# Kernel optimization log

Hardware: AMD Instinct MI355X
Metric: run time of the kernel (lower is better)

## Reference

```python
import jax, jax.numpy as jnp
import numpy as np

B, S, HID, H = 4, 2048, 1024, 16
D = HID // H  # dim per head


def setup_inputs() -> dict:
    key = jax.random.key(0)
    ks = jax.random.split(key, 7)
    inp = {
        "q": jax.random.normal(ks[0], (B, S, HID), dtype=jnp.float32),
        "k": jax.random.normal(ks[1], (B, S, HID), dtype=jnp.float32),
        "v": jax.random.normal(ks[2], (B, S, HID), dtype=jnp.float32),
        # Linear weights stored as (in, out); applied as x @ W. use_bias=False.
        "Wq": jax.random.normal(ks[3], (HID, HID), dtype=jnp.float32) * (1.0 / np.sqrt(HID)),
        "Wk": jax.random.normal(ks[4], (HID, HID), dtype=jnp.float32) * (1.0 / np.sqrt(HID)),
        "Wv": jax.random.normal(ks[5], (HID, HID), dtype=jnp.float32) * (1.0 / np.sqrt(HID)),
        "Wo": jax.random.normal(ks[6], (HID, HID), dtype=jnp.float32) * (1.0 / np.sqrt(HID)),
    }
    return inp


def reference(q, k, v, Wq, Wk, Wv, Wo):
    scale = 1.0 / jnp.sqrt(jnp.float32(D))
    # QKV projections, then split hidden into (H, D) heads (same layout as transpose_qkv)
    Q = (q @ Wq).reshape(B, S, H, D)
    K = (k @ Wk).reshape(B, S, H, D)
    V = (v @ Wv).reshape(B, S, H, D)
    # scaled dot-product attention: full [B,H,S,S] score matrix, softmax over keys
    attn_w = jnp.einsum("bqhd,bkhd->bhqk", Q, K) * scale
    attn_w = jax.nn.softmax(attn_w, axis=-1)
    # dropout rate is 0 (eval-mode / deterministic)
    O = jnp.einsum("bhqk,bkhd->bqhd", attn_w, V).reshape(B, S, HID)
    return O @ Wo
```

## Files before the change

### kernel.cpp

```cpp
#include <hip/hip_runtime.h>


typedef __attribute__((ext_vector_type(8))) short short8;
typedef __attribute__((ext_vector_type(4))) float float4v;

#if __has_builtin(__builtin_amdgcn_exp2f)
#define EXP2F(x) __builtin_amdgcn_exp2f(x)
#else
#define EXP2F(x) exp2f(x)
#endif

__device__ __forceinline__ unsigned short f2b(float x) {
  return (unsigned short)((__float_as_uint(x) + 0x8000u) >> 16);
}
__device__ __forceinline__ unsigned pk2f(float a, float b) {
  unsigned ua = __float_as_uint(a) + 0x8000u;
  unsigned ub = __float_as_uint(b) + 0x8000u;
  return __builtin_amdgcn_perm(ub, ua, 0x07060302);
}

typedef __attribute__((address_space(3))) unsigned int lds_uint;
typedef const __attribute__((address_space(1))) unsigned int gbl_uint;
__device__ __forceinline__ void stage16(const unsigned short* g, unsigned short* l) {
#if __has_builtin(__builtin_amdgcn_global_load_lds)
  __builtin_amdgcn_global_load_lds((gbl_uint*)g, (lds_uint*)l, 16, 0, 0);
#else
  *(uint4*)l = *(const uint4*)g;
#endif
}

__global__ __launch_bounds__(256) void conv_qkv(const float* __restrict__ q,
                                                const float* __restrict__ k,
                                                const float* __restrict__ v,
                                                unsigned short* __restrict__ ws,
                                                float qscale) {
  const int z = blockIdx.y;
  const float* src = z == 0 ? q : (z == 1 ? k : v);
  unsigned short* dst = ws + (size_t)z * 8388608;
  const float s = z == 0 ? qscale : 1.0f;
  size_t i = ((size_t)blockIdx.x * 256 + threadIdx.x) * 8;
  float4v a = *(const float4v*)(src + i);
  float4v b = *(const float4v*)(src + i + 4);
  uint4 o;
  o.x = pk2f(a.x * s, a.y * s);
  o.y = pk2f(a.z * s, a.w * s);
  o.z = pk2f(b.x * s, b.y * s);
  o.w = pk2f(b.z * s, b.w * s);
  *(uint4*)(dst + i) = o;
}

__global__ __launch_bounds__(256) void wtrans(const float* __restrict__ Wq,
                                              const float* __restrict__ Wk,
                                              const float* __restrict__ Wv,
                                              const float* __restrict__ Wo,
                                              unsigned short* __restrict__ Wt) {
  __shared__ float tile[32][33];
  const float* W = blockIdx.z == 0 ? Wq : blockIdx.z == 1 ? Wk
                   : blockIdx.z == 2 ? Wv : Wo;
  unsigned short* T = Wt + (size_t)blockIdx.z * 1048576;
  const int tx = threadIdx.x & 31, ty = threadIdx.x >> 5;
  const int k0 = blockIdx.y * 32, n0 = blockIdx.x * 32;
#pragma unroll
  for (int i = 0; i < 4; i++)
    tile[ty + 8 * i][tx] = W[(size_t)(k0 + ty + 8 * i) * 1024 + n0 + tx];
  __syncthreads();
#pragma unroll
  for (int i = 0; i < 4; i++)
    T[(size_t)(n0 + ty + 8 * i) * 1024 + k0 + tx] = f2b(tile[tx][ty + 8 * i]);
}

template <int MODE, bool SWAP>
__global__ __launch_bounds__(256, 2) void gemm_bt(const unsigned short* __restrict__ A,
                                                  const unsigned short* __restrict__ Bt,
                                                  void* __restrict__ Cg) {
  __shared__ __align__(16) unsigned short As[128 * 64];
  __shared__ __align__(16) unsigned short Bs[128 * 64];
  const int tid = threadIdx.x;
  const int lane = tid & 63;
  const int w = tid >> 6;
  const int quad = lane >> 4, col = lane & 15;
  const int wm = w >> 1, wn = w & 1;
  const int lin = blockIdx.x;
  const int xcd = lin & 7, grp = lin >> 3;
  const int m0 = ((grp & 7) * 8 + xcd) * 128;
  const int n0 = (grp >> 3) * 128;
  const int rA = lane >> 3, cA = lane & 7;

  float4v acc[4][4] = {};

  for (int k0 = 0; k0 < 1024; k0 += 64) {
    __syncthreads();
#pragma unroll
    for (int j = 0; j < 4; j++) {
      const int row = w * 32 + j * 8 + rA;
      stage16(A + (unsigned)(m0 + row) * 1024 + k0 + ((cA ^ rA) * 8),
              &As[row * 64 + cA * 8]);
      stage16(Bt + (unsigned)(n0 + row) * 1024 + k0 + ((cA ^ rA) * 8),
              &Bs[row * 64 + cA * 8]);
    }
    __syncthreads();

#pragma unroll
    for (int ks = 0; ks < 2; ks++) {
      short8 af[4], bf[4];
#pragma unroll
      for (int mi = 0; mi < 4; mi++) {
        int row = wm * 64 + mi * 16 + col;
        af[mi] = *(const short8*)&As[row * 64 + (((ks * 4 + quad) ^ (col & 7)) * 8)];
      }
#pragma unroll
      for (int ni = 0; ni < 4; ni++) {
        int row = wn * 64 + ni * 16 + col;
        bf[ni] = *(const short8*)&Bs[row * 64 + (((ks * 4 + quad) ^ (col & 7)) * 8)];
      }
#pragma unroll
      for (int mi = 0; mi < 4; mi++)
#pragma unroll
        for (int ni = 0; ni < 4; ni++) {
          if (SWAP)
            acc[ni][mi] = __builtin_amdgcn_mfma_f32_16x16x32_bf16(
                bf[ni], af[mi], acc[ni][mi], 0, 0, 0);
          else
            acc[mi][ni] = __builtin_amdgcn_mfma_f32_16x16x32_bf16(
                af[mi], bf[ni], acc[mi][ni], 0, 0, 0);
        }
    }
  }

  if (MODE == 0) {
#pragma unroll
    for (int ni = 0; ni < 4; ni++) {
      const int cg = n0 + wn * 64 + ni * 16 + quad * 4;
      const int h = cg >> 6, dlo = cg & 63;
#pragma unroll
      for (int mi = 0; mi < 4; mi++) {
        const int tok = m0 + wm * 64 + mi * 16 + col;
        const int b = tok >> 11, s = tok & 2047;
        uint2 pk;
        pk.x = pk2f(acc[ni][mi][0], acc[ni][mi][1]);
        pk.y = pk2f(acc[ni][mi][2], acc[ni][mi][3]);
        *(uint2*)((unsigned short*)Cg +
                  ((unsigned)((b * 16 + h) * 2048 + s) * 64 + dlo)) = pk;
      }
    }
  } else if (MODE == 1) {
#pragma unroll
    for (int mi = 0; mi < 4; mi++) {
      const int tok = m0 + wm * 64 + mi * 16 + quad * 4;
      const int b = tok >> 11, s = tok & 2047;
#pragma unroll
      for (int ni = 0; ni < 4; ni++) {
        const int cg = n0 + wn * 64 + ni * 16 + col;
        const int h = cg >> 6, d = cg & 63;
        uint2 pk;
        pk.x = pk2f(acc[mi][ni][0], acc[mi][ni][1]);
        pk.y = pk2f(acc[mi][ni][2], acc[mi][ni][3]);
        *(uint2*)((unsigned short*)Cg +
                  ((unsigned)((b * 16 + h) * 64 + d) * 2048 + s)) = pk;
      }
    }
  } else {
#pragma unroll
    for (int mi = 0; mi < 4; mi++) {
      const int row = m0 + wm * 64 + mi * 16 + quad * 4;
#pragma unroll
      for (int ni = 0; ni < 4; ni++) {
        const int cg = n0 + wn * 64 + ni * 16 + col;
#pragma unroll
        for (int r = 0; r < 4; r++)
          ((float*)Cg)[(unsigned)(row + r) * 1024 + cg] = acc[mi][ni][r];
      }
    }
  }
}

#define PSTR 160
__global__ __launch_bounds__(256, 2) void attn_kernel(
    const unsigned short* __restrict__ Qb, const unsigned short* __restrict__ Kb,
    const unsigned short* __restrict__ Vt, unsigned short* __restrict__ Ob) {
  __shared__ __align__(16) unsigned short K_lds[128 * 64];
  __shared__ __align__(16) unsigned short V_lds[64 * 128];
  __shared__ __align__(16) unsigned short P_lds[128 * PSTR];
  __shared__ float den_lds[128];

  const int tid = threadIdx.x;
  const int lane = tid & 63;
  const int w = tid >> 6;
  const int quad = lane >> 4, col = lane & 15;
  const int wq = w >> 1, wk = w & 1;
  const int lin = blockIdx.x;
  const int bh = ((lin >> 3) & 7) * 8 + (lin & 7);
  const int qt = lin >> 6;

  const unsigned short* Kbase = Kb + (size_t)bh * (2048 * 64);
  const unsigned short* Vbase = Vt + (size_t)bh * (64 * 2048);

  short8 qf[4][2];
#pragma unroll
  for (int qi = 0; qi < 4; qi++)
#pragma unroll
    for (int ks = 0; ks < 2; ks++) {
      int s = qt * 128 + wq * 64 + qi * 16 + col;
      qf[qi][ks] = *(const short8*)(Qb + ((size_t)bh * 2048 + s) * 64 + ks * 32 + quad * 8);
    }

  float4v oacc[2][4] = {};
  float dens[4] = {};

  if (tid < 128) den_lds[tid] = 0.f;

  const int rK = lane >> 3, cK = lane & 7;
  const int rV = lane >> 4, cV = lane & 15;

  for (int kt = 0; kt < 16; kt++) {
    const int s0 = kt * 128;
    __syncthreads();
#pragma unroll
    for (int j = 0; j < 4; j++) {
      const int rowK = w * 32 + j * 8 + rK;
      stage16(Kbase + (unsigned)(s0 + rowK) * 64 + ((cK ^ rK) * 8),
              &K_lds[rowK * 64 + cK * 8]);
      const int rowV = w * 16 + j * 4 + rV;
      stage16(Vbase + (unsigned)rowV * 2048 + s0 + (((cV ^ (rowV & 15)) & 15) * 8),
              &V_lds[rowV * 128 + cV * 8]);
    }
    __syncthreads();

    float4v sacc[4][4] = {};
    short8 kf[4][2];
#pragma unroll
    for (int ki = 0; ki < 4; ki++)
#pragma unroll
      for (int ks = 0; ks < 2; ks++) {
        int row = wk * 64 + ki * 16 + col;
        kf[ki][ks] = *(const short8*)&K_lds[row * 64 +
                                            (((ks * 4 + quad) ^ (col & 7)) * 8)];
      }
#pragma unroll
    for (int ki = 0; ki < 4; ki++)
#pragma unroll
      for (int qi = 0; qi < 4; qi++)
#pragma unroll
        for (int ks = 0; ks < 2; ks++)
          sacc[ki][qi] = __builtin_amdgcn_mfma_f32_16x16x32_bf16(
              kf[ki][ks], qf[qi][ks], sacc[ki][qi], 0, 0, 0);

#pragma unroll
    for (int ki = 0; ki < 4; ki++) {
      const int c = wk * 8 + ki * 2 + (quad >> 1);
      const int hh = quad & 1;
#pragma unroll
      for (int qi = 0; qi < 4; qi++) {
        const int q = wq * 64 + qi * 16 + col;
        float p0 = EXP2F(sacc[ki][qi][0]);
        float p1 = EXP2F(sacc[ki][qi][1]);
        float p2 = EXP2F(sacc[ki][qi][2]);
        float p3 = EXP2F(sacc[ki][qi][3]);
        dens[qi] += (p0 + p1) + (p2 + p3);
        uint2 pk;
        pk.x = pk2f(p0, p1);
        pk.y = pk2f(p2, p3);
        *(uint2*)&P_lds[q * PSTR + ((c ^ col) & 15) * 8 + hh * 4] = pk;
      }
    }
    __syncthreads();

#pragma unroll
    for (int ks = 0; ks < 4; ks++) {
      short8 pf[4], vf[2];
#pragma unroll
      for (int mi = 0; mi < 4; mi++) {
        int row = wq * 64 + mi * 16 + col;
        pf[mi] = *(const short8*)&P_lds[row * PSTR + ((((ks * 4 + quad) ^ col) & 15) * 8)];
      }
#pragma unroll
      for (int nv = 0; nv < 2; nv++) {
        int row = wk * 32 + nv * 16 + col;
        vf[nv] = *(const short8*)&V_lds[row * 128 + ((((ks * 4 + quad) ^ col) & 15) * 8)];
      }
#pragma unroll
      for (int nv = 0; nv < 2; nv++)
#pragma unroll
        for (int mi = 0; mi < 4; mi++)
          oacc[nv][mi] = __builtin_amdgcn_mfma_f32_16x16x32_bf16(
              vf[nv], pf[mi], oacc[nv][mi], 0, 0, 0);
    }
  }

#pragma unroll
  for (int qi = 0; qi < 4; qi++) {
    float v = dens[qi];
    v += __shfl_xor(v, 16);
    v += __shfl_xor(v, 32);
    if (lane < 16) atomicAdd(&den_lds[wq * 64 + qi * 16 + col], v);
  }
  __syncthreads();

  const int b = bh >> 4, h = bh & 15;
#pragma unroll
  for (int mi = 0; mi < 4; mi++) {
    const int srow = qt * 128 + wq * 64 + mi * 16 + col;
    const float rd = 1.f / den_lds[wq * 64 + mi * 16 + col];
    unsigned base = (unsigned)(b * 2048 + srow) * 1024 + h * 64;
#pragma unroll
    for (int nv = 0; nv < 2; nv++) {
      const int d0 = wk * 32 + nv * 16 + quad * 4;
      uint2 pk;
      pk.x = pk2f(oacc[nv][mi][0] * rd, oacc[nv][mi][1] * rd);
      pk.y = pk2f(oacc[nv][mi][2] * rd, oacc[nv][mi][3] * rd);
      *(uint2*)(Ob + base + d0) = pk;
    }
  }
}

extern "C" void kernel_launch(void* const* d_in, const int* in_sizes, int n_in,
                              void* d_out, int out_size, void* d_ws, size_t ws_size,
                              hipStream_t stream) {
  const float* q = (const float*)d_in[0];
  const float* k = (const float*)d_in[1];
  const float* v = (const float*)d_in[2];
  const float* Wq = (const float*)d_in[3];
  const float* Wk = (const float*)d_in[4];
  const float* Wv = (const float*)d_in[5];
  const float* Wo = (const float*)d_in[6];

  unsigned short* ws = (unsigned short*)d_ws;
  unsigned short* qb = ws;
  unsigned short* kb = ws + 8388608;
  unsigned short* vb = ws + 16777216;
  unsigned short* Qb = ws + 25165824;
  unsigned short* Kb = ws + 33554432;
  unsigned short* Vt = ws + 41943040;
  unsigned short* Wt = ws + 50331648;

  dim3 blk(256);
  const float qscale = 0.18033688011112042f;

  conv_qkv<<<dim3(4096, 3), blk, 0, stream>>>(q, k, v, ws, qscale);
  wtrans<<<dim3(32, 32, 4), blk, 0, stream>>>(Wq, Wk, Wv, Wo, Wt);

  gemm_bt<0, true><<<dim3(512), blk, 0, stream>>>(qb, Wt + 0 * 1048576, Qb);
  gemm_bt<0, true><<<dim3(512), blk, 0, stream>>>(kb, Wt + 1 * 1048576, Kb);
  gemm_bt<1, false><<<dim3(512), blk, 0, stream>>>(vb, Wt + 2 * 1048576, Vt);

  attn_kernel<<<dim3(1024), blk, 0, stream>>>(Qb, Kb, Vt, qb );

  gemm_bt<2, false><<<dim3(512), blk, 0, stream>>>(qb , Wt + 3 * 1048576,
                                                   (float*)d_out);
}
```

Before: 350.4 us.

## Rework attention to 32x32 MFMA with register-resident P and fuse QKV GEMMs

```diff
diff --git a/kernel.cpp b/kernel.cpp
--- a/kernel.cpp
+++ b/kernel.cpp
@@ -3,6 +3,7 @@
 
 typedef __attribute__((ext_vector_type(8))) short short8;
 typedef __attribute__((ext_vector_type(4))) float float4v;
+typedef __attribute__((ext_vector_type(16))) float float16v;
 
 #if __has_builtin(__builtin_amdgcn_exp2f)
 #define EXP2F(x) __builtin_amdgcn_exp2f(x)
@@ -69,10 +70,111 @@
     T[(size_t)(n0 + ty + 8 * i) * 1024 + k0 + tx] = f2b(tile[tx][ty + 8 * i]);
 }
 
-template <int MODE, bool SWAP>
-__global__ __launch_bounds__(256, 2) void gemm_bt(const unsigned short* __restrict__ A,
-                                                  const unsigned short* __restrict__ Bt,
-                                                  void* __restrict__ Cg) {
+__global__ __launch_bounds__(256, 3) void gemm_qkv(
+    const unsigned short* __restrict__ qb, const unsigned short* __restrict__ kb,
+    const unsigned short* __restrict__ vb, const unsigned short* __restrict__ Wt,
+    unsigned short* __restrict__ Qb, unsigned short* __restrict__ Kb,
+    unsigned short* __restrict__ Vt) {
+  __shared__ __align__(16) unsigned short As[128 * 64];
+  __shared__ __align__(16) unsigned short Bs[128 * 64];
+  const int tid = threadIdx.x;
+  const int lane = tid & 63;
+  const int w = tid >> 6;
+  const int quad = lane >> 4, col = lane & 15;
+  const int wm = w >> 1, wn = w & 1;
+  const int lin = blockIdx.x;
+  const int z = lin >> 9;
+  const int r = lin & 511;
+  const int xcd = r & 7, grp = r >> 3;
+  const int m0 = ((grp & 7) * 8 + xcd) * 128;
+  const int n0 = (grp >> 3) * 128;
+  const int rA = lane >> 3, cA = lane & 7;
+
+  const unsigned short* A = z == 0 ? qb : (z == 1 ? kb : vb);
+  const unsigned short* Bt = Wt + (unsigned)z * 1048576;
+
+  float4v acc[4][4] = {};
+
+  for (int k0 = 0; k0 < 1024; k0 += 64) {
+    __syncthreads();
+#pragma unroll
+    for (int j = 0; j < 4; j++) {
+      const int row = w * 32 + j * 8 + rA;
+      stage16(A + (unsigned)(m0 + row) * 1024 + k0 + ((cA ^ rA) * 8),
+              &As[row * 64 + cA * 8]);
+      stage16(Bt + (unsigned)(n0 + row) * 1024 + k0 + ((cA ^ rA) * 8),
+              &Bs[row * 64 + cA * 8]);
+    }
+    __syncthreads();
+
+#pragma unroll
+    for (int ks = 0; ks < 2; ks++) {
+      short8 af[4], bf[4];
+#pragma unroll
+      for (int mi = 0; mi < 4; mi++) {
+        int row = wm * 64 + mi * 16 + col;
+        af[mi] = *(const short8*)&As[row * 64 + (((ks * 4 + quad) ^ (col & 7)) * 8)];
+      }
+#pragma unroll
+      for (int ni = 0; ni < 4; ni++) {
+        int row = wn * 64 + ni * 16 + col;
+        bf[ni] = *(const short8*)&Bs[row * 64 + (((ks * 4 + quad) ^ (col & 7)) * 8)];
+      }
+      if (z < 2) {
+#pragma unroll
+        for (int mi = 0; mi < 4; mi++)
+#pragma unroll
+          for (int ni = 0; ni < 4; ni++)
+            acc[ni][mi] = __builtin_amdgcn_mfma_f32_16x16x32_bf16(
+                bf[ni], af[mi], acc[ni][mi], 0, 0, 0);
+      } else {
+#pragma unroll
+        for (int mi = 0; mi < 4; mi++)
+#pragma unroll
+          for (int ni = 0; ni < 4; ni++)
+            acc[mi][ni] = __builtin_amdgcn_mfma_f32_16x16x32_bf16(
+                af[mi], bf[ni], acc[mi][ni], 0, 0, 0);
+      }
+    }
+  }
+
+  if (z < 2) {
+    unsigned short* Cg = z == 0 ? Qb : Kb;
+#pragma unroll
+    for (int ni = 0; ni < 4; ni++) {
+      const int cg = n0 + wn * 64 + ni * 16 + quad * 4;
+      const int h = cg >> 6, dlo = cg & 63;
+#pragma unroll
+      for (int mi = 0; mi < 4; mi++) {
+        const int tok = m0 + wm * 64 + mi * 16 + col;
+        const int b = tok >> 11, s = tok & 2047;
+        uint2 pk;
+        pk.x = pk2f(acc[ni][mi][0], acc[ni][mi][1]);
+        pk.y = pk2f(acc[ni][mi][2], acc[ni][mi][3]);
+        *(uint2*)(Cg + ((unsigned)((b * 16 + h) * 2048 + s) * 64 + dlo)) = pk;
+      }
+    }
+  } else {
+#pragma unroll
+    for (int mi = 0; mi < 4; mi++) {
+      const int tok = m0 + wm * 64 + mi * 16 + quad * 4;
+      const int b = tok >> 11, s = tok & 2047;
+#pragma unroll
+      for (int ni = 0; ni < 4; ni++) {
+        const int cg = n0 + wn * 64 + ni * 16 + col;
+        const int h = cg >> 6, d = cg & 63;
+        uint2 pk;
+        pk.x = pk2f(acc[mi][ni][0], acc[mi][ni][1]);
+        pk.y = pk2f(acc[mi][ni][2], acc[mi][ni][3]);
+        *(uint2*)(Vt + ((unsigned)((b * 16 + h) * 64 + d) * 2048 + s)) = pk;
+      }
+    }
+  }
+}
+
+__global__ __launch_bounds__(256, 2) void gemm_out(const unsigned short* __restrict__ A,
+                                                   const unsigned short* __restrict__ Bt,
+                                                   float* __restrict__ Cg) {
   __shared__ __align__(16) unsigned short As[128 * 64];
   __shared__ __align__(16) unsigned short Bs[128 * 64];
   const int tid = threadIdx.x;
@@ -116,78 +218,37 @@
 #pragma unroll
       for (int mi = 0; mi < 4; mi++)
 #pragma unroll
-        for (int ni = 0; ni < 4; ni++) {
-          if (SWAP)
-            acc[ni][mi] = __builtin_amdgcn_mfma_f32_16x16x32_bf16(
-                bf[ni], af[mi], acc[ni][mi], 0, 0, 0);
-          else
-            acc[mi][ni] = __builtin_amdgcn_mfma_f32_16x16x32_bf16(
-                af[mi], bf[ni], acc[mi][ni], 0, 0, 0);
-        }
-    }
-  }
-
-  if (MODE == 0) {
+        for (int ni = 0; ni < 4; ni++)
+          acc[mi][ni] = __builtin_amdgcn_mfma_f32_16x16x32_bf16(af[mi], bf[ni],
+                                                               acc[mi][ni], 0, 0, 0);
+    }
+  }
+
+#pragma unroll
+  for (int mi = 0; mi < 4; mi++) {
+    const int row = m0 + wm * 64 + mi * 16 + quad * 4;
 #pragma unroll
     for (int ni = 0; ni < 4; ni++) {
-      const int cg = n0 + wn * 64 + ni * 16 + quad * 4;
-      const int h = cg >> 6, dlo = cg & 63;
-#pragma unroll
-      for (int mi = 0; mi < 4; mi++) {
-        const int tok = m0 + wm * 64 + mi * 16 + col;
-        const int b = tok >> 11, s = tok & 2047;
-        uint2 pk;
-        pk.x = pk2f(acc[ni][mi][0], acc[ni][mi][1]);
-        pk.y = pk2f(acc[ni][mi][2], acc[ni][mi][3]);
-        *(uint2*)((unsigned short*)Cg +
-                  ((unsigned)((b * 16 + h) * 2048 + s) * 64 + dlo)) = pk;
-      }
-    }
-  } else if (MODE == 1) {
-#pragma unroll
-    for (int mi = 0; mi < 4; mi++) {
-      const int tok = m0 + wm * 64 + mi * 16 + quad * 4;
-      const int b = tok >> 11, s = tok & 2047;
-#pragma unroll
-      for (int ni = 0; ni < 4; ni++) {
-        const int cg = n0 + wn * 64 + ni * 16 + col;
-        const int h = cg >> 6, d = cg & 63;
-        uint2 pk;
-        pk.x = pk2f(acc[mi][ni][0], acc[mi][ni][1]);
-        pk.y = pk2f(acc[mi][ni][2], acc[mi][ni][3]);
-        *(uint2*)((unsigned short*)Cg +
-                  ((unsigned)((b * 16 + h) * 64 + d) * 2048 + s)) = pk;
-      }
-    }
-  } else {
-#pragma unroll
-    for (int mi = 0; mi < 4; mi++) {
-      const int row = m0 + wm * 64 + mi * 16 + quad * 4;
-#pragma unroll
-      for (int ni = 0; ni < 4; ni++) {
-        const int cg = n0 + wn * 64 + ni * 16 + col;
-#pragma unroll
-        for (int r = 0; r < 4; r++)
-          ((float*)Cg)[(unsigned)(row + r) * 1024 + cg] = acc[mi][ni][r];
-      }
-    }
-  }
-}
-
-#define PSTR 160
-__global__ __launch_bounds__(256, 2) void attn_kernel(
+      const int cg = n0 + wn * 64 + ni * 16 + col;
+#pragma unroll
+      for (int r = 0; r < 4; r++)
+        Cg[(unsigned)(row + r) * 1024 + cg] = acc[mi][ni][r];
+    }
+  }
+}
+
+__global__ __launch_bounds__(256, 3) void attn_kernel(
     const unsigned short* __restrict__ Qb, const unsigned short* __restrict__ Kb,
     const unsigned short* __restrict__ Vt, unsigned short* __restrict__ Ob) {
   __shared__ __align__(16) unsigned short K_lds[128 * 64];
   __shared__ __align__(16) unsigned short V_lds[64 * 128];
-  __shared__ __align__(16) unsigned short P_lds[128 * PSTR];
-  __shared__ float den_lds[128];
 
   const int tid = threadIdx.x;
   const int lane = tid & 63;
   const int w = tid >> 6;
-  const int quad = lane >> 4, col = lane & 15;
-  const int wq = w >> 1, wk = w & 1;
+  const int l31 = lane & 31;
+  const int hl = lane >> 5;
+
   const int lin = blockIdx.x;
   const int bh = ((lin >> 3) & 7) * 8 + (lin & 7);
   const int qt = lin >> 6;
@@ -195,122 +256,108 @@
   const unsigned short* Kbase = Kb + (size_t)bh * (2048 * 64);
   const unsigned short* Vbase = Vt + (size_t)bh * (64 * 2048);
 
-  short8 qf[4][2];
-#pragma unroll
-  for (int qi = 0; qi < 4; qi++)
-#pragma unroll
-    for (int ks = 0; ks < 2; ks++) {
-      int s = qt * 128 + wq * 64 + qi * 16 + col;
-      qf[qi][ks] = *(const short8*)(Qb + ((size_t)bh * 2048 + s) * 64 + ks * 32 + quad * 8);
-    }
-
-  float4v oacc[2][4] = {};
-  float dens[4] = {};
-
-  if (tid < 128) den_lds[tid] = 0.f;
-
-  const int rK = lane >> 3, cK = lane & 7;
-  const int rV = lane >> 4, cV = lane & 15;
+  short8 qf[4];
+  {
+    const int s = qt * 128 + w * 32 + l31;
+    const unsigned short* qrow = Qb + ((size_t)bh * 2048 + s) * 64 + 8 * hl;
+#pragma unroll
+    for (int ks = 0; ks < 4; ks++) qf[ks] = *(const short8*)(qrow + 16 * ks);
+  }
+
+  float16v oacc[2];
+#pragma unroll
+  for (int di = 0; di < 2; di++)
+#pragma unroll
+    for (int e = 0; e < 16; e++) oacc[di][e] = 0.f;
+  float den = 0.f;
+
+  union PF { uint2 u[2]; short8 s8; };
 
   for (int kt = 0; kt < 16; kt++) {
     const int s0 = kt * 128;
     __syncthreads();
 #pragma unroll
-    for (int j = 0; j < 4; j++) {
-      const int rowK = w * 32 + j * 8 + rK;
-      stage16(Kbase + (unsigned)(s0 + rowK) * 64 + ((cK ^ rK) * 8),
-              &K_lds[rowK * 64 + cK * 8]);
-      const int rowV = w * 16 + j * 4 + rV;
-      stage16(Vbase + (unsigned)rowV * 2048 + s0 + (((cV ^ (rowV & 15)) & 15) * 8),
-              &V_lds[rowV * 128 + cV * 8]);
-    }
-    __syncthreads();
-
-    float4v sacc[4][4] = {};
-    short8 kf[4][2];
-#pragma unroll
-    for (int ki = 0; ki < 4; ki++)
-#pragma unroll
-      for (int ks = 0; ks < 2; ks++) {
-        int row = wk * 64 + ki * 16 + col;
-        kf[ki][ks] = *(const short8*)&K_lds[row * 64 +
-                                            (((ks * 4 + quad) ^ (col & 7)) * 8)];
-      }
-#pragma unroll
-    for (int ki = 0; ki < 4; ki++)
-#pragma unroll
-      for (int qi = 0; qi < 4; qi++)
-#pragma unroll
-        for (int ks = 0; ks < 2; ks++)
-          sacc[ki][qi] = __builtin_amdgcn_mfma_f32_16x16x32_bf16(
-              kf[ki][ks], qf[qi][ks], sacc[ki][qi], 0, 0, 0);
-
+    for (int jj = 0; jj < 4; jj++) {
+      {
+        const int row = (w * 4 + jj) * 8 + (lane >> 3);
+        const int cl = (lane & 7) ^ (row & 7);
+        stage16(Kbase + (unsigned)(s0 + row) * 64 + cl * 8,
+                &K_lds[row * 64 + (lane & 7) * 8]);
+      }
+      {
+        const int row = (w * 4 + jj) * 4 + (lane >> 4);
+        const int cl = (lane & 15) ^ (row & 15);
+        stage16(Vbase + (unsigned)row * 2048 + s0 + cl * 8,
+                &V_lds[row * 128 + (lane & 15) * 8]);
+      }
+    }
+    __syncthreads();
+
+    PF pfrag[8];
 #pragma unroll
     for (int ki = 0; ki < 4; ki++) {
-      const int c = wk * 8 + ki * 2 + (quad >> 1);
-      const int hh = quad & 1;
-#pragma unroll
-      for (int qi = 0; qi < 4; qi++) {
-        const int q = wq * 64 + qi * 16 + col;
-        float p0 = EXP2F(sacc[ki][qi][0]);
-        float p1 = EXP2F(sacc[ki][qi][1]);
-        float p2 = EXP2F(sacc[ki][qi][2]);
-        float p3 = EXP2F(sacc[ki][qi][3]);
-        dens[qi] += (p0 + p1) + (p2 + p3);
-        uint2 pk;
-        pk.x = pk2f(p0, p1);
-        pk.y = pk2f(p2, p3);
-        *(uint2*)&P_lds[q * PSTR + ((c ^ col) & 15) * 8 + hh * 4] = pk;
-      }
-    }
-    __syncthreads();
-
-#pragma unroll
-    for (int ks = 0; ks < 4; ks++) {
-      short8 pf[4], vf[2];
-#pragma unroll
-      for (int mi = 0; mi < 4; mi++) {
-        int row = wq * 64 + mi * 16 + col;
-        pf[mi] = *(const short8*)&P_lds[row * PSTR + ((((ks * 4 + quad) ^ col) & 15) * 8)];
-      }
-#pragma unroll
-      for (int nv = 0; nv < 2; nv++) {
-        int row = wk * 32 + nv * 16 + col;
-        vf[nv] = *(const short8*)&V_lds[row * 128 + ((((ks * 4 + quad) ^ col) & 15) * 8)];
-      }
-#pragma unroll
-      for (int nv = 0; nv < 2; nv++)
-#pragma unroll
-        for (int mi = 0; mi < 4; mi++)
-          oacc[nv][mi] = __builtin_amdgcn_mfma_f32_16x16x32_bf16(
-              vf[nv], pf[mi], oacc[nv][mi], 0, 0, 0);
-    }
-  }
-
-#pragma unroll
-  for (int qi = 0; qi < 4; qi++) {
-    float v = dens[qi];
-    v += __shfl_xor(v, 16);
-    v += __shfl_xor(v, 32);
-    if (lane < 16) atomicAdd(&den_lds[wq * 64 + qi * 16 + col], v);
-  }
-  __syncthreads();
+      float16v sacc;
+#pragma unroll
+      for (int e = 0; e < 16; e++) sacc[e] = 0.f;
+#pragma unroll
+      for (int ks = 0; ks < 4; ks++) {
+        const int row = ki * 32 + l31;
+        short8 kfr = *(const short8*)&K_lds[row * 64 +
+                                            (((2 * ks + hl) ^ (row & 7)) * 8)];
+        sacc = __builtin_amdgcn_mfma_f32_32x32x16_bf16(kfr, qf[ks], sacc, 0, 0, 0);
+      }
+      uint2 u2[4];
+#pragma unroll
+      for (int g = 0; g < 4; g++) {
+        float p0 = EXP2F(sacc[4 * g + 0]);
+        float p1 = EXP2F(sacc[4 * g + 1]);
+        float p2 = EXP2F(sacc[4 * g + 2]);
+        float p3 = EXP2F(sacc[4 * g + 3]);
+        den += (p0 + p1) + (p2 + p3);
+        u2[g].x = pk2f(p0, p1);
+        u2[g].y = pk2f(p2, p3);
+      }
+#pragma unroll
+      for (int pz = 0; pz < 2; pz++) {
+        const uint2 own = u2[2 * pz + hl];
+        const uint2 snd = u2[2 * pz + 1 - hl];
+        uint2 rec;
+        rec.x = (unsigned)__shfl_xor((int)snd.x, 32);
+        rec.y = (unsigned)__shfl_xor((int)snd.y, 32);
+        pfrag[2 * ki + pz].u[0] = hl ? rec : own;
+        pfrag[2 * ki + pz].u[1] = hl ? own : rec;
+      }
+    }
+
+#pragma unroll
+    for (int ks = 0; ks < 8; ks++) {
+#pragma unroll
+      for (int di = 0; di < 2; di++) {
+        const int row = di * 32 + l31;
+        short8 vfr = *(const short8*)&V_lds[row * 128 +
+                                            (((2 * ks + hl) ^ (row & 15)) * 8)];
+        oacc[di] = __builtin_amdgcn_mfma_f32_32x32x16_bf16(vfr, pfrag[ks].s8,
+                                                           oacc[di], 0, 0, 0);
+      }
+    }
+  }
+
+  den += __shfl_xor(den, 32);
+  const float rd = 1.f / den;
 
   const int b = bh >> 4, h = bh & 15;
-#pragma unroll
-  for (int mi = 0; mi < 4; mi++) {
-    const int srow = qt * 128 + wq * 64 + mi * 16 + col;
-    const float rd = 1.f / den_lds[wq * 64 + mi * 16 + col];
-    unsigned base = (unsigned)(b * 2048 + srow) * 1024 + h * 64;
-#pragma unroll
-    for (int nv = 0; nv < 2; nv++) {
-      const int d0 = wk * 32 + nv * 16 + quad * 4;
+  const int s = qt * 128 + w * 32 + l31;
+  const unsigned base = (unsigned)(b * 2048 + s) * 1024 + h * 64;
+#pragma unroll
+  for (int di = 0; di < 2; di++)
+#pragma unroll
+    for (int g = 0; g < 4; g++) {
+      const int d0 = di * 32 + 8 * g + 4 * hl;
       uint2 pk;
-      pk.x = pk2f(oacc[nv][mi][0] * rd, oacc[nv][mi][1] * rd);
-      pk.y = pk2f(oacc[nv][mi][2] * rd, oacc[nv][mi][3] * rd);
+      pk.x = pk2f(oacc[di][4 * g + 0] * rd, oacc[di][4 * g + 1] * rd);
+      pk.y = pk2f(oacc[di][4 * g + 2] * rd, oacc[di][4 * g + 3] * rd);
       *(uint2*)(Ob + base + d0) = pk;
     }
-  }
 }
 
 extern "C" void kernel_launch(void* const* d_in, const int* in_sizes, int n_in,
@@ -339,12 +386,10 @@
   conv_qkv<<<dim3(4096, 3), blk, 0, stream>>>(q, k, v, ws, qscale);
   wtrans<<<dim3(32, 32, 4), blk, 0, stream>>>(Wq, Wk, Wv, Wo, Wt);
 
-  gemm_bt<0, true><<<dim3(512), blk, 0, stream>>>(qb, Wt + 0 * 1048576, Qb);
-  gemm_bt<0, true><<<dim3(512), blk, 0, stream>>>(kb, Wt + 1 * 1048576, Kb);
-  gemm_bt<1, false><<<dim3(512), blk, 0, stream>>>(vb, Wt + 2 * 1048576, Vt);
+  gemm_qkv<<<dim3(1536), blk, 0, stream>>>(qb, kb, vb, Wt, Qb, Kb, Vt);
 
   attn_kernel<<<dim3(1024), blk, 0, stream>>>(Qb, Kb, Vt, qb );
 
-  gemm_bt<2, false><<<dim3(512), blk, 0, stream>>>(qb , Wt + 3 * 1048576,
-                                                   (float*)d_out);
-}
+  gemm_out<<<dim3(512), blk, 0, stream>>>(qb , Wt + 3 * 1048576,
+                                          (float*)d_out);
+}
```

Measured after the change: 480.8 us. +37.2%, slower.
